# Kernel optimization log

Measured on AMD Instinct MI355X. Metric: run time of the kernel, lower is better.

## Reference

```python
import jax, jax.numpy as jnp
import numpy as np

BLOCK_SIZE = 64
NUM_STEPS = 3
# pad_type='post', init_type='ones', attention_mask=None


def setup_inputs() -> dict:
    key = jax.random.key(0)
    k1, k2, k3 = jax.random.split(key, 3)
    B, H, S, D = 4, 16, 4096, 64
    return {
        "query": jax.random.normal(k1, (B, H, S, D), dtype=jnp.float32),
        "key": jax.random.normal(k2, (B, H, S, D), dtype=jnp.float32),
        "value": jax.random.normal(k3, (B, H, S, D), dtype=jnp.float32),
    }


def _soba_monarch(query, key, value):
    B, H, S, D = query.shape
    bs = BLOCK_SIZE
    nb = -(-S // bs)                 # ceil(S / bs)
    pad = nb * bs - S                # post padding amount
    q = query / (D ** 0.5)

    pad_cfg = ((0, 0), (0, 0), (0, pad), (0, 0))
    Qb = jnp.pad(q, pad_cfg).reshape(B, H, nb, bs, D)      # (l j) v -> l j v
    Kb = jnp.pad(key, pad_cfg).reshape(B, H, nb, bs, D)    # (k i) v -> k i v

    # validity of positions in the padded sequence (post-pad)
    pos_valid = (jnp.arange(nb * bs) < S).reshape(nb, bs)  # [block, within]
    # left factor shape (..., j, l, k): rows of the flattened (l j) axis
    left_mask = jnp.broadcast_to(pos_valid.T[:, :, None], (bs, nb, nb))      # j l k
    # right factor shape (..., k, j, i): columns of the flattened (k i) axis
    right_mask = jnp.broadcast_to(pos_valid[:, None, :], (nb, bs, bs))       # k j i

    NEG = jnp.finfo(q.dtype).min
    # init_type = 'ones'
    left = jnp.broadcast_to(
        jnp.where(left_mask, 1.0 / nb, 0.0), (B, H, bs, nb, nb)
    ).astype(q.dtype)

    for _ in range(NUM_STEPS):
        # beta[k,j,i] = sum_{l,v} left[j,l,k] Q[l,j,v] K[k,i,v]
        beta = jnp.einsum('bhjlk,bhljv,bhkiv->bhkji', left, Qb, Kb, optimize=True)
        tau = jnp.swapaxes(jnp.sum(left, axis=-2), -1, -2)[..., None]        # bhkj1
        tau_zero = jnp.isclose(tau, 0.0)
        tau_safe = jnp.where(tau_zero, 1.0, tau)
        logits_r = jnp.where(right_mask & ~tau_zero, beta / tau_safe, NEG)
        right = jax.nn.softmax(logits_r, axis=-1)
        right = jnp.where(right_mask, right, 0.0)

        # alpha[j,1,k] = sum_i right[k,j,i] log right[k,j,i]  (xlogy)
        r_safe = jnp.where(right > 0, right, 1.0)
        alpha = jnp.sum(right * jnp.log(r_safe), axis=-1)                    # bhkj
        alpha = jnp.swapaxes(alpha, -1, -2)[..., None, :]                    # bhj1k

        beta2 = jnp.einsum('bhkji,bhljv,bhkiv->bhjlk', right, Qb, Kb, optimize=True)
        left = jax.nn.softmax(jnp.where(left_mask, beta2 - alpha, NEG), axis=-1)
        left = jnp.where(left_mask, left, 0.0)

    # multiply: z = L (R V)
    Vb = jnp.pad(value, pad_cfg).reshape(B, H, nb, bs, D)                    # k i v
    Y = jnp.einsum('bhkji,bhkiv->bhkjv', right, Vb)
    Z = jnp.einsum('bhjlk,bhkjv->bhljv', left, Y)
    z = Z.reshape(B, H, nb * bs, D)
    return z[..., :S, :]


def reference(query, key, value):
    return _soba_monarch(query, key, value)
```

## Files before the change

kernel.cpp:

```cpp
#include <hip/hip_runtime.h>


namespace {

typedef __attribute__((ext_vector_type(8))) short short8v;
typedef __attribute__((ext_vector_type(4))) float f32x4;

constexpr int HEADS = 64;
constexpr size_t HEADQ = 262144;
constexpr size_t MATF  = (size_t)HEADS * 262144;

#define MFMA(ACC, A, B) ACC = __builtin_amdgcn_mfma_f32_16x16x32_bf16(A, B, ACC, 0, 0, 0)

__device__ __forceinline__ void gload16(const ushort* g, ushort* l) {
    __builtin_amdgcn_global_load_lds(
        (const __attribute__((address_space(1))) void*)g,
        (__attribute__((address_space(3))) void*)l, 16, 0, 0);
}

__device__ __forceinline__ int swz(int row, int col) {
    return row * 64 + (((col >> 3) ^ (row & 7)) << 3) + (col & 7);
}
__device__ __forceinline__ short8v ldx(const ushort* a, int row, int chunk) {
    return *(const short8v*)(a + row * 64 + ((chunk ^ (row & 7)) << 3));
}

__device__ __forceinline__ void bfsplit(float x, ushort& h, ushort& l) {
    uint u = __float_as_uint(x);
    uint hi = (u + 0x7FFFu + ((u >> 16) & 1u)) & 0xFFFF0000u;
    h = (ushort)(hi >> 16);
    l = (ushort)(__float_as_uint(x - __uint_as_float(hi)) >> 16);
}

struct Frag16 { short8v h0, h1, l0, l1; };

__device__ __forceinline__ Frag16 split_load(const float* __restrict__ p, float s) {
    Frag16 f;
    #pragma unroll
    for (int q = 0; q < 4; ++q) {
        float4 a = *(const float4*)(p + 4 * q);
        float v[4] = {a.x * s, a.y * s, a.z * s, a.w * s};
        #pragma unroll
        for (int e = 0; e < 4; ++e) {
            ushort hh, ll; bfsplit(v[e], hh, ll);
            const int i = 4 * q + e;
            if (i < 8) { f.h0[i] = (short)hh; f.l0[i] = (short)ll; }
            else       { f.h1[i - 8] = (short)hh; f.l1[i - 8] = (short)ll; }
        }
    }
    return f;
}
__device__ __forceinline__ void store_rows(ushort* H, ushort* L, int r, int c0,
                                           const Frag16& f) {
    const int ch = c0 >> 3;
    const int o0 = r * 64 + ((ch ^ (r & 7)) << 3);
    const int o1 = r * 64 + (((ch + 1) ^ (r & 7)) << 3);
    *(short8v*)(H + o0) = f.h0; *(short8v*)(H + o1) = f.h1;
    *(short8v*)(L + o0) = f.l0; *(short8v*)(L + o1) = f.l1;
}
__device__ __forceinline__ void scatter_tr(ushort* H, ushort* L, int r, int c0,
                                           const Frag16& f) {
    #pragma unroll
    for (int e = 0; e < 8; ++e) {
        H[swz(c0 + e, r)] = (ushort)f.h0[e];
        L[swz(c0 + e, r)] = (ushort)f.l0[e];
    }
    #pragma unroll
    for (int e = 0; e < 8; ++e) {
        H[swz(c0 + 8 + e, r)] = (ushort)f.h1[e];
        L[swz(c0 + 8 + e, r)] = (ushort)f.l1[e];
    }
}

__device__ __forceinline__ void flush8k(const ushort* S, ushort* g, int tid) {
    *(short8v*)(g + tid * 8)        = *(const short8v*)(S + tid * 8);
    *(short8v*)(g + 2048 + tid * 8) = *(const short8v*)(S + 2048 + tid * 8);
}

__device__ __forceinline__ void mmstep(const ushort* AH, const ushort* AL,
                                       const ushort* BH, const ushort* BL,
                                       int w, int lo4, int hi4, f32x4 acc[4]) {
    #pragma unroll
    for (int ks = 0; ks < 2; ++ks) {
        short8v ah = ldx(AH, 16 * w + lo4, hi4 + 4 * ks);
        short8v al = ldx(AL, 16 * w + lo4, hi4 + 4 * ks);
        #pragma unroll
        for (int t = 0; t < 4; ++t) {
            short8v bh = ldx(BH, 16 * t + lo4, hi4 + 4 * ks);
            short8v bl = ldx(BL, 16 * t + lo4, hi4 + 4 * ks);
            MFMA(acc[t], ah, bh); MFMA(acc[t], ah, bl); MFMA(acc[t], al, bh);
        }
    }
}
__device__ __forceinline__ void mmstep_swap(const ushort* AH, const ushort* AL,
                                            const ushort* BH, const ushort* BL,
                                            int w, int lo4, int hi4, f32x4 acc[4]) {
    #pragma unroll
    for (int ks = 0; ks < 2; ++ks) {
        short8v bh = ldx(AH, 16 * w + lo4, hi4 + 4 * ks);
        short8v bl = ldx(AL, 16 * w + lo4, hi4 + 4 * ks);
        #pragma unroll
        for (int m = 0; m < 4; ++m) {
            short8v ah = ldx(BH, 16 * m + lo4, hi4 + 4 * ks);
            short8v al = ldx(BL, 16 * m + lo4, hi4 + 4 * ks);
            MFMA(acc[m], ah, bh); MFMA(acc[m], ah, bl); MFMA(acc[m], al, bh);
        }
    }
}

__device__ __forceinline__ float max16(const float* x) {
    float a = fmaxf(fmaxf(x[0], x[1]), fmaxf(x[2], x[3]));
    float b = fmaxf(fmaxf(x[4], x[5]), fmaxf(x[6], x[7]));
    float c = fmaxf(fmaxf(x[8], x[9]), fmaxf(x[10], x[11]));
    float d = fmaxf(fmaxf(x[12], x[13]), fmaxf(x[14], x[15]));
    return fmaxf(fmaxf(a, b), fmaxf(c, d));
}

__global__ __launch_bounds__(256) void kmean_kernel(const float* __restrict__ Q,
                                                    ushort* __restrict__ Mh,
                                                    ushort* __restrict__ Ml) {
    const int wg = blockIdx.x;
    const int h  = wg >> 4;
    const int j  = ((wg & 15) << 2) + (threadIdx.x >> 6);
    const int v  = threadIdx.x & 63;
    const float* base = Q + (size_t)h * HEADQ + (size_t)j * 64 + v;
    float acc = 0.f;
    #pragma unroll
    for (int l = 0; l < 64; ++l) acc += base[(size_t)l * 4096];
    ushort hh, ll; bfsplit(acc * (1.0f / 512.0f), hh, ll);
    const int idx = swz(j, v);
    Mh[(size_t)h * 4096 + idx] = hh;
    Ml[(size_t)h * 4096 + idx] = ll;
}

template<int FIRST, int LAST>
__global__ __launch_bounds__(256, 4) void bc_kernel(
    const ushort* __restrict__ Gh,
    const ushort* __restrict__ Gl,
    const float*  __restrict__ Kmat,
    const float*  __restrict__ Vmat,
    const float*  __restrict__ tauIn,
    ushort* __restrict__ Hmh,
    ushort* __restrict__ Hml,
    float*  __restrict__ alphaOut,
    ushort* __restrict__ Yh,
    ushort* __restrict__ Yl)
{
    __shared__ __align__(16) ushort SM[16384];
    ushort* Ah = SM;          ushort* Al = SM + 4096;
    ushort* Bh = SM + 8192;   ushort* Bl = SM + 12288;

    const int wg = blockIdx.x, h = wg >> 6, k = wg & 63;
    const int tid = threadIdx.x, r = tid & 63, c0 = (tid >> 6) << 4;
    const int w = tid >> 6, lo4 = tid & 15, hi4 = (tid >> 4) & 3;

    #pragma unroll
    for (int a = 0; a < 2; ++a) {
        const int o = a * 4096 + tid * 16;
        size_t src;
        if (FIRST) {
            src = (size_t)h * 4096 + (size_t)(o >> 1);
        } else {
            const int row = o >> 7, cd = (o >> 4) & 7;
            const int cu = cd ^ (row & 7);
            src = ((size_t)h * 64 + row) * 4096 + (size_t)k * 64
                + (size_t)((cu ^ (k & 7)) << 3);
        }
        gload16(Gh + src, (ushort*)((char*)Ah + o));
        gload16(Gl + src, (ushort*)((char*)Al + o));
    }
    Frag16 fk = split_load(Kmat + (size_t)h * HEADQ + (size_t)k * 4096 + r * 64 + c0, 1.f);
    store_rows(Bh, Bl, r, c0, fk);
    Frag16 fv;
    if (LAST)
        fv = split_load(Vmat + (size_t)h * HEADQ + (size_t)k * 4096 + r * 64 + c0, 1.f);
    float tv = 1.f;
    if (!FIRST) tv = tauIn[((size_t)h * 64 + k) * 64 + 16 * w + lo4];
    __syncthreads();

    f32x4 acc[4] = {};
    mmstep_swap(Ah, Al, Bh, Bl, w, lo4, hi4, acc);
    __syncthreads();

    {
        const int j = 16 * w + lo4;
        const bool tz = !(tv > 1e-8f);
        const float tvi = tz ? 1.f : 1.f / tv;
        float x[16];
        #pragma unroll
        for (int m = 0; m < 4; ++m)
            #pragma unroll
            for (int rg = 0; rg < 4; ++rg) x[4 * m + rg] = acc[m][rg] * tvi;
        float mx = max16(x);
        mx = fmaxf(mx, __shfl_xor(mx, 16));
        mx = fmaxf(mx, __shfl_xor(mx, 32));
        float ex[16], s = 0.f, p = 0.f;
        #pragma unroll
        for (int e = 0; e < 16; ++e) {
            ex[e] = __expf(x[e] - mx);
            s += ex[e];
            p = fmaf(ex[e], x[e], p);
        }
        s += __shfl_xor(s, 16);
        s += __shfl_xor(s, 32);
        p += __shfl_xor(p, 16);
        p += __shfl_xor(p, 32);
        const float inv = 1.f / s;
        const float ap = tz ? -4.1588830834f
                            : fmaf(p, inv, -mx - __logf(s));
        #pragma unroll
        for (int m = 0; m < 4; ++m) {
            #pragma unroll
            for (int rg = 0; rg < 4; ++rg) {
                const float rv = tz ? (1.f / 64.f) : ex[4 * m + rg] * inv;
                ushort hh, ll; bfsplit(rv, hh, ll);
                const int idx = swz(j, 16 * m + 4 * hi4 + rg);
                Ah[idx] = hh; Al[idx] = ll;
            }
        }
        if (hi4 == 0) alphaOut[((size_t)h * 64 + j) * 64 + k] = ap;
    }
    scatter_tr(Bh, Bl, r, c0, fk);
    __syncthreads();

    f32x4 acc2[4] = {};
    mmstep(Ah, Al, Bh, Bl, w, lo4, hi4, acc2);
    const size_t ob = ((size_t)h * 64 + k) * 4096;
    if (!LAST) {
        __syncthreads();
        #pragma unroll
        for (int rr = 0; rr < 4; ++rr) {
            const int j = 16 * w + 4 * hi4 + rr;
            #pragma unroll
            for (int t = 0; t < 4; ++t) {
                ushort hh, ll; bfsplit(acc2[t][rr], hh, ll);
                const int idx = swz(j, 16 * t + lo4);
                Bh[idx] = hh; Bl[idx] = ll;
            }
        }
        __syncthreads();
        flush8k(Bh, Hmh + ob, tid);
        flush8k(Bl, Hml + ob, tid);
    } else {
        __syncthreads();
        scatter_tr(Bh, Bl, r, c0, fv);
        __syncthreads();
        f32x4 acc3[4] = {};
        mmstep(Ah, Al, Bh, Bl, w, lo4, hi4, acc3);
        __syncthreads();
        #pragma unroll
        for (int rr = 0; rr < 4; ++rr) {
            const int j = 16 * w + 4 * hi4 + rr;
            #pragma unroll
            for (int t = 0; t < 4; ++t) {
                const int idx = swz(j, 16 * t + lo4);
                ushort hh, ll;
                bfsplit(acc2[t][rr], hh, ll);
                Ah[idx] = hh; Al[idx] = ll;
                bfsplit(acc3[t][rr], hh, ll);
                Bh[idx] = hh; Bl[idx] = ll;
            }
        }
        __syncthreads();
        flush8k(Ah, Hmh + ob, tid);
        flush8k(Al, Hml + ob, tid);
        flush8k(Bh, Yh + ob, tid);
        flush8k(Bl, Yl + ob, tid);
    }
}

template<int LAST>
__global__ __launch_bounds__(256, 4) void da_kernel(
    const float*  __restrict__ Q,
    const ushort* __restrict__ Hmh,
    const ushort* __restrict__ Hml,
    const float*  __restrict__ alphaIn,
    const ushort* __restrict__ Yh,
    const ushort* __restrict__ Yl,
    ushort* __restrict__ Goh,
    ushort* __restrict__ Gol,
    float*  __restrict__ tauOut,
    float*  __restrict__ Zout)
{
    __shared__ __align__(16) ushort SM[16384];
    ushort* Ah = SM;          ushort* Al = SM + 4096;
    ushort* Bh = SM + 8192;   ushort* Bl = SM + 12288;
    float* OSZ = (float*)(SM + 8192);

    const int wg = blockIdx.x, h = wg >> 6, j = wg & 63;
    const int tid = threadIdx.x, r = tid & 63, c0 = (tid >> 6) << 4;
    const int w = tid >> 6, lo4 = tid & 15, hi4 = (tid >> 4) & 3;

    #pragma unroll
    for (int a = 0; a < 2; ++a) {
        const int o = a * 4096 + tid * 16;
        const int kd = o >> 7, cd = (o >> 4) & 7;
        const int cu = cd ^ (kd & 7);
        const size_t src = ((size_t)h * 64 + kd) * 4096 + (size_t)j * 64
                         + (size_t)((cu ^ (j & 7)) << 3);
        gload16(Hmh + src, (ushort*)((char*)Bh + o));
        gload16(Hml + src, (ushort*)((char*)Bl + o));
    }
    Frag16 fq = split_load(Q + (size_t)h * HEADQ + (size_t)r * 4096 + (size_t)j * 64 + c0,
                           0.125f);
    store_rows(Ah, Al, r, c0, fq);
    Frag16 fy;
    if (LAST) {
        const size_t yb = ((size_t)h * 64 + r) * 4096 + (size_t)j * 64;
        const int ch = c0 >> 3;
        const int sA = ((ch ^ (j & 7)) << 3), sB = (((ch + 1) ^ (j & 7)) << 3);
        fy.h0 = *(const short8v*)(Yh + yb + sA);
        fy.h1 = *(const short8v*)(Yh + yb + sB);
        fy.l0 = *(const short8v*)(Yl + yb + sA);
        fy.l1 = *(const short8v*)(Yl + yb + sB);
    }
    float av[16];
    {
        const float* ap0 = alphaIn + ((size_t)h * 64 + j) * 64 + 4 * hi4;
        #pragma unroll
        for (int m = 0; m < 4; ++m)
            #pragma unroll
            for (int rg = 0; rg < 4; ++rg) av[4 * m + rg] = ap0[16 * m + rg];
    }
    __syncthreads();

    f32x4 acc[4] = {};
    mmstep_swap(Ah, Al, Bh, Bl, w, lo4, hi4, acc);
    __syncthreads();

    {
        const int l = 16 * w + lo4;
        float x[16];
        #pragma unroll
        for (int m = 0; m < 4; ++m)
            #pragma unroll
            for (int rg = 0; rg < 4; ++rg) x[4 * m + rg] = acc[m][rg] - av[4 * m + rg];
        float mx = max16(x);
        mx = fmaxf(mx, __shfl_xor(mx, 16));
        mx = fmaxf(mx, __shfl_xor(mx, 32));
        #pragma unroll
        for (int e = 0; e < 16; ++e) x[e] = __expf(x[e] - mx);
        float s = 0.f;
        #pragma unroll
        for (int e = 0; e < 16; ++e) s += x[e];
        s += __shfl_xor(s, 16);
        s += __shfl_xor(s, 32);
        const float inv = 1.f / s;
        #pragma unroll
        for (int m = 0; m < 4; ++m) {
            #pragma unroll
            for (int rg = 0; rg < 4; ++rg) {
                const float lv = x[4 * m + rg] * inv;
                ushort hh, ll; bfsplit(lv, hh, ll);
                const int kk = 16 * m + 4 * hi4 + rg;
                const int idx = LAST ? swz(l, kk) : swz(kk, l);
                Bh[idx] = hh; Bl[idx] = ll;
            }
        }
    }
    if (!LAST) scatter_tr(Ah, Al, r, c0, fq);
    else       scatter_tr(Ah, Al, r, c0, fy);
    __syncthreads();

    if (!LAST) {
        f32x4 acc2[4] = {};
        f32x4 tacc = {};
        short8v onesb;
        #pragma unroll
        for (int e2 = 0; e2 < 8; ++e2) onesb[e2] = (lo4 == 0) ? (short)0x3F80 : (short)0;
        #pragma unroll
        for (int ks = 0; ks < 2; ++ks) {
            short8v ah = ldx(Bh, 16 * w + lo4, hi4 + 4 * ks);
            short8v al = ldx(Bl, 16 * w + lo4, hi4 + 4 * ks);
            MFMA(tacc, ah, onesb); MFMA(tacc, al, onesb);
            #pragma unroll
            for (int t = 0; t < 4; ++t) {
                short8v bh = ldx(Ah, 16 * t + lo4, hi4 + 4 * ks);
                short8v bl = ldx(Al, 16 * t + lo4, hi4 + 4 * ks);
                MFMA(acc2[t], ah, bh); MFMA(acc2[t], ah, bl); MFMA(acc2[t], al, bh);
            }
        }
        __syncthreads();
        #pragma unroll
        for (int rr = 0; rr < 4; ++rr) {
            const int kq = 16 * w + 4 * hi4 + rr;
            if (lo4 == 0) tauOut[((size_t)h * 64 + kq) * 64 + j] = tacc[rr];
            #pragma unroll
            for (int t = 0; t < 4; ++t) {
                ushort hh, ll; bfsplit(acc2[t][rr], hh, ll);
                const int idx = swz(kq, 16 * t + lo4);
                Bh[idx] = hh; Bl[idx] = ll;
            }
        }
        __syncthreads();
        const size_t ob = ((size_t)h * 64 + j) * 4096;
        flush8k(Bh, Goh + ob, tid);
        flush8k(Bl, Gol + ob, tid);
    } else {
        f32x4 acc2[4] = {};
        #pragma unroll
        for (int ks = 0; ks < 2; ++ks) {
            short8v ah = ldx(Bh, 16 * w + lo4, hi4 + 4 * ks);
            short8v al = ldx(Bl, 16 * w + lo4, hi4 + 4 * ks);
            #pragma unroll
            for (int t = 0; t < 4; ++t) {
                short8v bh = ldx(Ah, 16 * t + lo4, hi4 + 4 * ks);
                short8v bl = ldx(Al, 16 * t + lo4, hi4 + 4 * ks);
                MFMA(acc2[t], ah, bh); MFMA(acc2[t], ah, bl); MFMA(acc2[t], al, bh);
            }
        }
        __syncthreads();
        #pragma unroll
        for (int rr = 0; rr < 4; ++rr) {
            const int l = 16 * w + 4 * hi4 + rr;
            #pragma unroll
            for (int t = 0; t < 4; ++t) OSZ[l * 64 + 16 * t + lo4] = acc2[t][rr];
        }
        __syncthreads();
        #pragma unroll
        for (int q = 0; q < 4; ++q) {
            const int lrow = (tid >> 4) + 16 * q;
            const int v4 = (tid & 15) * 4;
            float4 vv = *(const float4*)(OSZ + lrow * 64 + v4);
            *(float4*)(Zout + (size_t)h * HEADQ + (size_t)lrow * 4096 + (size_t)j * 64 + v4) = vv;
        }
    }
}

}

extern "C" void kernel_launch(void* const* d_in, const int* in_sizes, int n_in,
                              void* d_out, int out_size, void* d_ws, size_t ws_size,
                              hipStream_t stream) {
    const float* Q = (const float*)d_in[0];
    const float* K = (const float*)d_in[1];
    const float* V = (const float*)d_in[2];
    float* out = (float*)d_out;

    char* ws = (char*)d_ws;
    const size_t MB = 1024 * 1024;
    ushort* Gh  = (ushort*)(ws);
    ushort* Gl  = (ushort*)(ws + 32 * MB);
    ushort* Hmh = (ushort*)(ws + 64 * MB);
    ushort* Hml = (ushort*)(ws + 96 * MB);
    ushort* Mh  = (ushort*)(ws + 128 * MB);
    ushort* Ml  = (ushort*)(ws + 128 * MB + 512 * 1024);
    float*  al  = (float*)(ws + 129 * MB);
    float*  tau = (float*)(ws + 130 * MB);

    const bool bigws = ws_size >= (size_t)195 * MB;
    ushort* Yh = bigws ? (ushort*)(ws + 131 * MB) : (ushort*)out;
    ushort* Yl = bigws ? (ushort*)(ws + 163 * MB) : (ushort*)out + 16777216;
    float*  Zdst = bigws ? out : (float*)ws;

    dim3 blk(256), grid(HEADS * 64);

    kmean_kernel<<<dim3(1024), blk, 0, stream>>>(Q, Mh, Ml);
    bc_kernel<1, 0><<<grid, blk, 0, stream>>>(Mh, Ml, K, nullptr, nullptr,
                                              Hmh, Hml, al, nullptr, nullptr);
    da_kernel<0>   <<<grid, blk, 0, stream>>>(Q, Hmh, Hml, al, nullptr, nullptr,
                                              Gh, Gl, tau, nullptr);
    bc_kernel<0, 0><<<grid, blk, 0, stream>>>(Gh, Gl, K, nullptr, tau,
                                              Hmh, Hml, al, nullptr, nullptr);
    da_kernel<0>   <<<grid, blk, 0, stream>>>(Q, Hmh, Hml, al, nullptr, nullptr,
                                              Gh, Gl, tau, nullptr);
    bc_kernel<0, 1><<<grid, blk, 0, stream>>>(Gh, Gl, K, V, tau,
                                              Hmh, Hml, al, Yh, Yl);
    da_kernel<1>   <<<grid, blk, 0, stream>>>(Q, Hmh, Hml, al, Yh, Yl,
                                              nullptr, nullptr, nullptr, Zdst);
    if (!bigws)
        hipMemcpyAsync(d_out, Zdst, MATF * sizeof(float), hipMemcpyDeviceToDevice, stream);
}
```

Baseline: 300.5 us.

## Write intermediate matrices pre-transposed so consumers load contiguous tiles

The producer kernels now scatter their bf16 hi/lo results directly to global memory in the layout the consumer kernel needs: row j, block k, swizzled. Previously they staged through LDS and flushed contiguous 8 KB tiles, and the consumer gathered strided 16-byte chunks. The consumers can now issue contiguous global-to-LDS loads, and the producer drops its LDS staging and barriers. The cost is that the producer's global writes become 2-byte scattered stores spread across many rows, which may coalesce poorly.

```diff
diff --git a/kernel.cpp b/kernel.cpp
--- a/kernel.cpp
+++ b/kernel.cpp
@@ -157,15 +157,8 @@
     #pragma unroll
     for (int a = 0; a < 2; ++a) {
         const int o = a * 4096 + tid * 16;
-        size_t src;
-        if (FIRST) {
-            src = (size_t)h * 4096 + (size_t)(o >> 1);
-        } else {
-            const int row = o >> 7, cd = (o >> 4) & 7;
-            const int cu = cd ^ (row & 7);
-            src = ((size_t)h * 64 + row) * 4096 + (size_t)k * 64
-                + (size_t)((cu ^ (k & 7)) << 3);
-        }
+        const size_t src = FIRST ? ((size_t)h * 4096 + (size_t)(o >> 1))
+                                 : (((size_t)h * 64 + k) * 4096 + (size_t)(o >> 1));
         gload16(Gh + src, (ushort*)((char*)Ah + o));
         gload16(Gl + src, (ushort*)((char*)Al + o));
     }
@@ -225,45 +218,36 @@
 
     f32x4 acc2[4] = {};
     mmstep(Ah, Al, Bh, Bl, w, lo4, hi4, acc2);
-    const size_t ob = ((size_t)h * 64 + k) * 4096;
-    if (!LAST) {
+    #pragma unroll
+    for (int rr = 0; rr < 4; ++rr) {
+        const int j = 16 * w + 4 * hi4 + rr;
+        const size_t tb = ((size_t)h * 64 + j) * 4096;
+        #pragma unroll
+        for (int t = 0; t < 4; ++t) {
+            ushort hh, ll; bfsplit(acc2[t][rr], hh, ll);
+            const int idx = swz(k, 16 * t + lo4);
+            Hmh[tb + idx] = hh; Hml[tb + idx] = ll;
+        }
+    }
+    if (LAST) {
+        __syncthreads();
+        scatter_tr(Bh, Bl, r, c0, fv);
+        __syncthreads();
+        f32x4 acc3[4] = {};
+        mmstep(Ah, Al, Bh, Bl, w, lo4, hi4, acc3);
         __syncthreads();
         #pragma unroll
         for (int rr = 0; rr < 4; ++rr) {
             const int j = 16 * w + 4 * hi4 + rr;
             #pragma unroll
             for (int t = 0; t < 4; ++t) {
-                ushort hh, ll; bfsplit(acc2[t][rr], hh, ll);
+                ushort hh, ll; bfsplit(acc3[t][rr], hh, ll);
                 const int idx = swz(j, 16 * t + lo4);
                 Bh[idx] = hh; Bl[idx] = ll;
             }
         }
         __syncthreads();
-        flush8k(Bh, Hmh + ob, tid);
-        flush8k(Bl, Hml + ob, tid);
-    } else {
-        __syncthreads();
-        scatter_tr(Bh, Bl, r, c0, fv);
-        __syncthreads();
-        f32x4 acc3[4] = {};
-        mmstep(Ah, Al, Bh, Bl, w, lo4, hi4, acc3);
-        __syncthreads();
-        #pragma unroll
-        for (int rr = 0; rr < 4; ++rr) {
-            const int j = 16 * w + 4 * hi4 + rr;
-            #pragma unroll
-            for (int t = 0; t < 4; ++t) {
-                const int idx = swz(j, 16 * t + lo4);
-                ushort hh, ll;
-                bfsplit(acc2[t][rr], hh, ll);
-                Ah[idx] = hh; Al[idx] = ll;
-                bfsplit(acc3[t][rr], hh, ll);
-                Bh[idx] = hh; Bl[idx] = ll;
-            }
-        }
-        __syncthreads();
-        flush8k(Ah, Hmh + ob, tid);
-        flush8k(Al, Hml + ob, tid);
+        const size_t ob = ((size_t)h * 64 + k) * 4096;
         flush8k(Bh, Yh + ob, tid);
         flush8k(Bl, Yl + ob, tid);
     }
@@ -294,10 +278,7 @@
     #pragma unroll
     for (int a = 0; a < 2; ++a) {
         const int o = a * 4096 + tid * 16;
-        const int kd = o >> 7, cd = (o >> 4) & 7;
-        const int cu = cd ^ (kd & 7);
-        const size_t src = ((size_t)h * 64 + kd) * 4096 + (size_t)j * 64
-                         + (size_t)((cu ^ (j & 7)) << 3);
+        const size_t src = ((size_t)h * 64 + j) * 4096 + (size_t)(o >> 1);
         gload16(Hmh + src, (ushort*)((char*)Bh + o));
         gload16(Hml + src, (ushort*)((char*)Bl + o));
     }
@@ -380,22 +361,18 @@
                 MFMA(acc2[t], ah, bh); MFMA(acc2[t], ah, bl); MFMA(acc2[t], al, bh);
             }
         }
-        __syncthreads();
         #pragma unroll
         for (int rr = 0; rr < 4; ++rr) {
             const int kq = 16 * w + 4 * hi4 + rr;
             if (lo4 == 0) tauOut[((size_t)h * 64 + kq) * 64 + j] = tacc[rr];
+            const size_t tb = ((size_t)h * 64 + kq) * 4096;
             #pragma unroll
             for (int t = 0; t < 4; ++t) {
                 ushort hh, ll; bfsplit(acc2[t][rr], hh, ll);
-                const int idx = swz(kq, 16 * t + lo4);
-                Bh[idx] = hh; Bl[idx] = ll;
-            }
-        }
-        __syncthreads();
-        const size_t ob = ((size_t)h * 64 + j) * 4096;
-        flush8k(Bh, Goh + ob, tid);
-        flush8k(Bl, Gol + ob, tid);
+                const int idx = swz(j, 16 * t + lo4);
+                Goh[tb + idx] = hh; Gol[tb + idx] = ll;
+            }
+        }
     } else {
         f32x4 acc2[4] = {};
         #pragma unroll
```

New measurement: 312.5 us. 1.04x slower.
